# Performance work log

Hardware: AMD Instinct MI355X
Metric: run time of the kernel (lower is better)

The kernel has to match this reference:

```python
import jax, jax.numpy as jnp
import numpy as np

K = 16
EPS = 1e-5
SLOPE = 0.2


def knn_idx(k, xyz_k, xyz_q):
    # xyz_k: (B,Nk,3), xyz_q: (B,Nq,3) -> (B,Nq,k) indices of k nearest in xyz_k
    d = (jnp.sum(xyz_q * xyz_q, -1, keepdims=True)
         - 2.0 * jnp.einsum('bqc,bkc->bqk', xyz_q, xyz_k)
         + jnp.sum(xyz_k * xyz_k, -1)[:, None, :])
    _, idx = jax.lax.top_k(-d, k)
    return idx


def graph_feature(coor_q, x_q, coor_k, x_k):
    # coor_*: (B,N*,3); x_q: (B,C,Nq); x_k: (B,C,Nk) -> (B,2C,Nq,K)
    idx = knn_idx(K, coor_k, coor_q)                      # (B,Nq,K)
    nbr = jax.vmap(lambda xk, i: xk[:, i])(x_k, idx)       # (B,C,Nq,K)
    xq = x_q[:, :, :, None]                                # (B,C,Nq,1)
    xq = jnp.broadcast_to(xq, nbr.shape)
    return jnp.concatenate([nbr - xq, xq], axis=1)


def group_norm(x, gamma, beta, groups=4):
    B, C, N, Kk = x.shape
    xg = x.reshape(B, groups, C // groups, N, Kk)
    mu = jnp.mean(xg, axis=(2, 3, 4), keepdims=True)
    var = jnp.var(xg, axis=(2, 3, 4), keepdims=True)
    xn = ((xg - mu) / jnp.sqrt(var + EPS)).reshape(B, C, N, Kk)
    return xn * gamma[None, :, None, None] + beta[None, :, None, None]


def cgl(f, W, gamma, beta):
    # 1x1 Conv2d (no bias) + GroupNorm(4) + LeakyReLU(0.2)
    y = jnp.einsum('oc,bcnk->bonk', W, f)
    return jax.nn.leaky_relu(group_norm(y, gamma, beta), SLOPE)


def fps(xyz, m):
    # furthest point sampling. xyz: (B,N,3) -> (B,m) int32
    B, N, _ = xyz.shape
    first = jnp.zeros((B,), jnp.int32)

    def body(carry, _):
        dist, last = carry
        lp = jnp.take_along_axis(xyz, last[:, None, None].astype(jnp.int32), axis=1)  # (B,1,3)
        d = jnp.sum((xyz - lp) ** 2, -1)
        dist = jnp.minimum(dist, d)
        nxt = jnp.argmax(dist, -1).astype(jnp.int32)
        return (dist, nxt), nxt

    init = (jnp.full((B, N), 1e10, jnp.float32), first)
    _, rest = jax.lax.scan(body, init, None, length=m - 1)  # (m-1,B)
    return jnp.concatenate([first[None, :], rest], axis=0).T  # (B,m)


def fps_downsample(coor, x, m):
    # coor: (B,N,3), x: (B,C,N) -> new_coor (B,3,m), new_x (B,C,m)
    idx = fps(coor, m)                                        # (B,m)
    new_coor = jnp.take_along_axis(coor, idx[:, :, None], axis=1).transpose(0, 2, 1)
    new_x = jnp.take_along_axis(x, idx[:, None, :], axis=2)
    return new_coor, new_x


def setup_inputs() -> dict:
    key = jax.random.key(0)
    ks = jax.random.split(key, 16)
    d = {
        'x': jax.random.normal(ks[0], (8, 4096, 3), jnp.float32),
        'num0': 2048, 'num1': 512, 'num2': 128,
        'w_in': jax.random.normal(ks[1], (8, 3), jnp.float32) * 0.3,
        'b_in': jnp.zeros((8,), jnp.float32),
    }
    layer_dims = {'1': (32, 16), '2': (64, 64), '4': (128, 128),
                  '5': (128, 256), '6': (256, 256), '7': (256, 512)}
    for i, (name, (o, c)) in enumerate(layer_dims.items()):
        d[f'w{name}'] = jax.random.normal(ks[2 + i], (o, c), jnp.float32) * (1.0 / np.sqrt(c))
        d[f'g{name}'] = jnp.ones((o,), jnp.float32)
        d[f'be{name}'] = jnp.zeros((o,), jnp.float32)
    return d


def reference(x, num0, num1, num2, w_in, b_in,
              w1, g1, be1, w2, g2, be2, w4, g4, be4,
              w5, g5, be5, w6, g6, be6, w7, g7, be7):
    xyz = x.transpose(0, 2, 1)                                # (B,3,N)
    coor = x                                                  # (B,N,3)
    f = jnp.einsum('oc,bcn->bon', w_in, xyz) + b_in[None, :, None]  # (B,8,N)

    f = cgl(graph_feature(coor, f, coor, f), w1, g1, be1)     # (B,32,N,K)
    f = jnp.max(f, axis=-1)                                   # (B,32,N)

    sp1, f_q = fps_downsample(coor, f, num0)                  # (B,3,n0),(B,32,n0)
    coor_d = sp1.transpose(0, 2, 1)                           # (B,n0,3)
    f = cgl(graph_feature(coor_d, f_q, coor, f), w2, g2, be2)
    stage1_feature = jnp.max(f, axis=-1)                      # (B,64,n0)
    coor = coor_d

    sp2, f_q = fps_downsample(coor, stage1_feature, num1)
    coor_d = sp2.transpose(0, 2, 1)
    f = cgl(graph_feature(coor_d, f_q, coor, stage1_feature), w4, g4, be4)
    f = jnp.max(f, axis=-1)                                   # (B,128,n1)
    f = cgl(graph_feature(coor_d, f, coor_d, f), w5, g5, be5)
    stage2_feature = jnp.max(f, axis=-1)                      # (B,128,n1)
    coor = coor_d

    sp3, f_q = fps_downsample(coor, stage2_feature, num2)
    coor_d = sp3.transpose(0, 2, 1)
    f = cgl(graph_feature(coor_d, f_q, coor, stage2_feature), w6, g6, be6)
    f = jnp.max(f, axis=-1)                                   # (B,256,n2)
    f = cgl(graph_feature(coor_d, f, coor_d, f), w7, g7, be7)
    stage3_feature = jnp.max(f, axis=-1)                      # (B,256,n2)

    out_coor = sp3.transpose(0, 2, 1)                         # (B,n2,3)
    out_f = stage3_feature.transpose(0, 2, 1)                 # (B,n2,256)
    return out_coor, out_f
```

## Files before the change

kernel.cpp:

```cpp
#include <hip/hip_runtime.h>
#include <hip/hip_bf16.h>
#include <math.h>

#define DEVI __device__ __forceinline__
typedef unsigned long long ull;

__global__ void k_feat0(const float* __restrict__ x,
                        const float* __restrict__ w_in,
                        const float* __restrict__ b_in,
                        float* __restrict__ coords0, float* __restrict__ feat0,
                        float* __restrict__ stats)
{
  int t = blockIdx.x*blockDim.x + threadIdx.x;
  if (t < 384) stats[t] = 0.f;
  if (t >= 8*4096) return;
  float cx = x[t*3+0], cy = x[t*3+1], cz = x[t*3+2];
  coords0[t*3+0]=cx; coords0[t*3+1]=cy; coords0[t*3+2]=cz;
  #pragma unroll
  for (int o=0;o<8;o++){
    float s = __fadd_rn(__fadd_rn(__fmul_rn(cx,w_in[o*3+0]),
                                  __fmul_rn(cy,w_in[o*3+1])),
                        __fmul_rn(cz,w_in[o*3+2]));
    feat0[t*8+o] = __fadd_rn(s, b_in[o]);
  }
}

template<int CTRL>
DEVI void dppmax64(unsigned& hi, unsigned& lo){
  unsigned oh = (unsigned)__builtin_amdgcn_update_dpp((int)hi,(int)hi,CTRL,0xF,0xF,false);
  unsigned ol = (unsigned)__builtin_amdgcn_update_dpp((int)lo,(int)lo,CTRL,0xF,0xF,false);
  bool tk = (oh > hi) || (oh == hi && ol > lo);
  hi = tk?oh:hi; lo = tk?ol:lo;
}

template<int P>
DEVI void fps_stage(float (&px)[P], float (&py)[P], float (&pz)[P],
                    int m, float sx, float sy, float sz,
                    const float* cpx, const float* cpy, const float* cpz,
                    ull* mK,
                    int* ssel, float* snx, float* sny, float* snz, int tid)
{
  const int wv = tid>>6, lane = tid&63;
  float dist[P];
  #pragma unroll
  for (int p=0;p<P;p++) dist[p]=1e10f;
  if (tid==0){ ssel[0]=0; if (snx){ snx[0]=sx; sny[0]=sy; snz[0]=sz; } }
  #pragma unroll 1
  for (int it=1; it<m; it++){
    float bv = -1.f;
    #pragma unroll
    for (int p=0;p<P;p++){
      float dx=__fsub_rn(px[p],sx);
      float dy=__fsub_rn(py[p],sy);
      float dz=__fsub_rn(pz[p],sz);
      float d = __fadd_rn(__fadd_rn(__fmul_rn(dx,dx),__fmul_rn(dy,dy)),
                          __fmul_rn(dz,dz));
      d = fminf(dist[p], d);
      dist[p] = d;
      bv = fmaxf(bv, d);
    }
    int bidx = 0;
    #pragma unroll
    for (int p=P-1;p>=0;p--) if (dist[p]==bv) bidx = tid+(p<<8);
    const unsigned itu = (unsigned)it;
    unsigned hi = __float_as_uint(bv);
    unsigned lo = ((~(unsigned)bidx & 0xFFFu)<<12) | itu;
    dppmax64<0x111>(hi,lo);
    dppmax64<0x112>(hi,lo);
    dppmax64<0x114>(hi,lo);
    dppmax64<0x118>(hi,lo);
    dppmax64<0x142>(hi,lo);
    dppmax64<0x143>(hi,lo);
    ull* slot = mK + ((it&1)<<2);
    if (lane==63)
      *(volatile ull*)(slot + wv) = ((ull)hi<<32) | (ull)lo;
    ull k0,k1,k2,k3;
    for (;;){
      asm volatile("" ::: "memory");
      k0=slot[0]; k1=slot[1]; k2=slot[2]; k3=slot[3];
      unsigned chk = (((unsigned)k0 ^ itu) | ((unsigned)k1 ^ itu) |
                      ((unsigned)k2 ^ itu) | ((unsigned)k3 ^ itu)) & 0xFFFu;
      if (chk == 0u) break;
    }
    ull ka = (k1>k0)?k1:k0;
    ull kb = (k3>k2)?k3:k2;
    ull kw = (kb>ka)?kb:ka;
    int gi = (int)((~((unsigned)(kw & 0xffffffffull) >> 12)) & 0xFFFu);
    sx = cpx[gi]; sy = cpy[gi]; sz = cpz[gi];
    if (tid==0){
      ssel[it]=gi;
      if (snx){ snx[it]=sx; sny[it]=sy; snz[it]=sz; }
    }
  }
}

template<int CTRL>
DEVI void dppmin_fj(float& d, int& j){
  float od = __int_as_float(__builtin_amdgcn_update_dpp(__float_as_int(d),__float_as_int(d),CTRL,0xF,0xF,false));
  int   oj = __builtin_amdgcn_update_dpp(j,j,CTRL,0xF,0xF,false);
  bool tk = (od < d) || (od == d && oj < j);
  d = tk?od:d; j = tk?oj:j;
}

DEVI float dist_qk(const float* __restrict__ ckb, int j,
                   float qx, float qy, float qz, float sqq){
  float kx=ckb[3*j], ky=ckb[3*j+1], kz=ckb[3*j+2];
  float sk  = __fadd_rn(__fadd_rn(__fmul_rn(kx,kx),__fmul_rn(ky,ky)),
                        __fmul_rn(kz,kz));
  float dot = __fadd_rn(__fadd_rn(__fmul_rn(qx,kx),__fmul_rn(qy,ky)),
                        __fmul_rn(qz,kz));
  return __fadd_rn(__fsub_rn(sqq, __fmul_rn(2.0f,dot)), sk);
}

template<int NPL>
DEVI void knn_wave(const float* __restrict__ cq, int Nq,
                   const float* __restrict__ ck, int Nk,
                   int* __restrict__ idx_out, int b, int q, int lane)
{
  size_t r3 = ((size_t)b*Nq+q)*3;
  float qx=cq[r3], qy=cq[r3+1], qz=cq[r3+2];
  float sqq = __fadd_rn(__fadd_rn(__fmul_rn(qx,qx),__fmul_rn(qy,qy)),
                        __fmul_rn(qz,qz));
  constexpr int GS = (NPL < 8) ? NPL : 8;
  constexpr int NG = NPL / GS;
  float gv[NG]; int gj[NG];
  const float* ckb = ck + (size_t)b*Nk*3;
  ull exmask = 0;
  int dirtyg = -1;
  int myout = 0;
  #pragma unroll 1
  for (int r=0; r<16; r++){
    #pragma unroll
    for (int g=0; g<NG; g++){
      if (dirtyg < 0 || dirtyg == g){
        float nv=__int_as_float(0x7f800000); int nj=0x7fffffff;
        #pragma unroll
        for (int e=0; e<GS; e++){
          const int i = g*GS+e;
          int j = lane + (i<<6);
          float d = dist_qk(ckb, j, qx,qy,qz, sqq);
          bool rem = ((exmask >> i) & 1ull) == 0ull;
          if (rem && d < nv){ nv=d; nj=j; }
        }
        gv[g]=nv; gj[g]=nj;
      }
    }
    float lv = gv[0]; int lj = gj[0];
    #pragma unroll
    for (int g=1; g<NG; g++)
      if (gv[g]<lv || (gv[g]==lv && gj[g]<lj)){ lv=gv[g]; lj=gj[g]; }
    float rd = lv; int rj = lj;
    dppmin_fj<0x111>(rd,rj);
    dppmin_fj<0x112>(rd,rj);
    dppmin_fj<0x114>(rd,rj);
    dppmin_fj<0x118>(rd,rj);
    dppmin_fj<0x142>(rd,rj);
    dppmin_fj<0x143>(rd,rj);
    int wj = __builtin_amdgcn_readlane(rj,63);
    if (lane == r) myout = wj;
    if ((wj & 63) == lane) exmask |= (1ull << (wj>>6));
    dirtyg = (wj>>6)/GS;
  }
  if (lane<16) idx_out[((size_t)b*Nq+q)*16 + lane] = myout;
}

template<int NPL>
__global__ __launch_bounds__(256,3) void k_knn_t(const float* __restrict__ cq, int Nq,
                                                 const float* __restrict__ ck, int Nk,
                                                 int* __restrict__ idx_out)
{
  const int b = blockIdx.y;
  const int q = blockIdx.x*4 + (threadIdx.x>>6);
  if (q >= Nq) return;
  knn_wave<NPL>(cq, Nq, ck, Nk, idx_out, b, q, threadIdx.x&63);
}

__global__ __launch_bounds__(256) void k_fps_knn1(
    const float* __restrict__ coords0,
    int* __restrict__ idx1, int* __restrict__ idx2, int* __restrict__ idx3,
    float* __restrict__ c1, float* __restrict__ c2, float* __restrict__ c3,
    float* __restrict__ out, int* __restrict__ knn1)
{
  __shared__ float s1x[4096], s1y[4096], s1z[4096];
  __shared__ float s2x[2048], s2y[2048], s2z[2048];
  __shared__ float s3x[512],  s3y[512],  s3z[512];
  __shared__ float s4x[128],  s4y[128],  s4z[128];
  __shared__ int   ssel[2048];
  __shared__ alignas(32) ull mK[8];
  if (blockIdx.x >= 8){
    int flat = blockIdx.x - 8;
    int b = flat >> 10, qb = flat & 1023;
    int q = qb*4 + (threadIdx.x>>6);
    knn_wave<64>(coords0, 4096, coords0, 4096, knn1, b, q, threadIdx.x&63);
    return;
  }
  const int b = blockIdx.x, tid = threadIdx.x;
  __builtin_amdgcn_s_setprio(3);
  const float* cb = coords0 + (size_t)b*4096*3;
  if (tid<8) mK[tid] = ~0ull;
  {
    float px[16], py[16], pz[16];
    #pragma unroll
    for (int p=0;p<16;p++){
      int j = tid + (p<<8);
      float X=cb[3*j], Y=cb[3*j+1], Z=cb[3*j+2];
      px[p]=X; py[p]=Y; pz[p]=Z;
      s1x[j]=X; s1y[j]=Y; s1z[j]=Z;
    }
    float sx=cb[0], sy=cb[1], sz=cb[2];
    __syncthreads();
    fps_stage<16>(px,py,pz, 2048, sx,sy,sz, s1x,s1y,s1z,
                  mK, ssel, s2x,s2y,s2z, tid);
  }
  __syncthreads();
  {
    float* c1b = c1 + (size_t)b*2048*3;
    for (int i=tid;i<2048;i+=256){
      idx1[b*2048+i]=ssel[i];
      c1b[3*i]=s2x[i]; c1b[3*i+1]=s2y[i]; c1b[3*i+2]=s2z[i];
    }
  }
  {
    float px[8], py[8], pz[8];
    #pragma unroll
    for (int p=0;p<8;p++){
      int j = tid + (p<<8);
      px[p]=s2x[j]; py[p]=s2y[j]; pz[p]=s2z[j];
    }
    float sx=s2x[0], sy=s2y[0], sz=s2z[0];
    __syncthreads();
    fps_stage<8>(px,py,pz, 512, sx,sy,sz, s2x,s2y,s2z,
                 mK, ssel, s3x,s3y,s3z, tid);
  }
  __syncthreads();
  {
    float* c2b = c2 + (size_t)b*512*3;
    for (int i=tid;i<512;i+=256){
      idx2[b*512+i]=ssel[i];
      c2b[3*i]=s3x[i]; c2b[3*i+1]=s3y[i]; c2b[3*i+2]=s3z[i];
    }
  }
  {
    float px[2], py[2], pz[2];
    #pragma unroll
    for (int p=0;p<2;p++){
      int j = tid + (p<<8);
      px[p]=s3x[j]; py[p]=s3y[j]; pz[p]=s3z[j];
    }
    float sx=s3x[0], sy=s3y[0], sz=s3z[0];
    __syncthreads();
    fps_stage<2>(px,py,pz, 128, sx,sy,sz, s3x,s3y,s3z,
                 mK, ssel, s4x,s4y,s4z, tid);
  }
  __syncthreads();
  {
    float* c3b = c3 + (size_t)b*128*3;
    float* ob  = out + (size_t)b*128*3;
    for (int i=tid;i<128;i+=256){
      idx3[b*128+i]=ssel[i];
      float X=s4x[i],Y=s4y[i],Z=s4z[i];
      c3b[3*i]=X; c3b[3*i+1]=Y; c3b[3*i+2]=Z;
      ob[3*i]=X; ob[3*i+1]=Y; ob[3*i+2]=Z;
    }
  }
}

struct WtParams {
  const float* W[6];
  float* wl[6];
  float* wq[6];
  int O[6], C[6], OC[6];
};
__global__ void k_wt_all(WtParams p){
  int s = blockIdx.y;
  int t = blockIdx.x*blockDim.x + threadIdx.x;
  int OC = p.OC[s];
  if (t >= OC) return;
  int C = p.C[s], O = p.O[s];
  int o = t / C, c = t - o*C;
  const float* W = p.W[s];
  float wlv = W[o*2*C + c];
  float wrv = W[o*2*C + C + c];
  p.wl[s][c*O+o] = wlv;
  p.wq[s][c*O+o] = wrv - wlv;
}

#define GEMM_M 8
__global__ void k_gemm_dual(const float* __restrict__ feat, int Nk, int C, int O,
                            const float* __restrict__ wlT, const float* __restrict__ wqT,
                            float* __restrict__ yk, float* __restrict__ yq)
{
  extern __shared__ float sf[];
  const int b = blockIdx.y;
  const int o = threadIdx.x & (O-1);
  const int rg = threadIdx.x / O;
  const int R = blockDim.x / O;
  const int rowsPB = R*GEMM_M;
  const int row0 = blockIdx.x * rowsPB;
  const int Cp = C+1;
  const float* src = feat + ((size_t)b*Nk + row0)*C;
  for (int i=threadIdx.x; i<rowsPB*C; i+=blockDim.x){
    int r = i / C, c = i - r*C;
    sf[r*Cp + c] = src[i];
  }
  __syncthreads();
  float ak[GEMM_M], aq[GEMM_M];
  #pragma unroll
  for (int m=0;m<GEMM_M;m++){ ak[m]=0.f; aq[m]=0.f; }
  const float* lp = wlT + o;
  const float* qp = wqT + o;
  const float* sfr = sf + rg*GEMM_M*Cp;
  for (int c=0;c<C;c++){
    float wl = lp[(size_t)c*O];
    float wq = qp[(size_t)c*O];
    #pragma unroll
    for (int m=0;m<GEMM_M;m++){
      float xv = sfr[m*Cp + c];
      ak[m] = fmaf(xv, wl, ak[m]);
      aq[m] = fmaf(xv, wq, aq[m]);
    }
  }
  size_t obase = ((size_t)b*Nk + row0 + rg*GEMM_M)*O + o;
  #pragma unroll
  for (int m=0;m<GEMM_M;m++){
    yk[obase + (size_t)m*O] = ak[m];
    yq[obase + (size_t)m*O] = aq[m];
  }
}

__global__ void k_gather(const float* __restrict__ yk, const float* __restrict__ yq,
                         const int* __restrict__ knnidx, const int* __restrict__ qmap,
                         int Nq, int Nk, int O,
                         float* __restrict__ vmax, float* __restrict__ stats)
{
  const int b = blockIdx.y;
  const int o = threadIdx.x & (O-1);
  const int rg = threadIdx.x / O;
  const int R = blockDim.x / O;
  float ls=0.f, ls2=0.f;
  const float* ykb = yk + (size_t)b*Nk*O;
  const float* yqb = yq + (size_t)b*Nk*O;
  for (int nq = blockIdx.x*R + rg; nq < Nq; nq += gridDim.x*R){
    int qj = qmap ? qmap[b*Nq+nq] : nq;
    float vq = yqb[(size_t)qj*O + o];
    const int* ip = knnidx + ((size_t)b*Nq+nq)*16;
    float vmx = -3.4e38f;
    #pragma unroll
    for (int k=0;k<16;k++){
      int j = ip[k];
      float v = ykb[(size_t)j*O+o] + vq;
      vmx = fmaxf(vmx, v);
      ls += v; ls2 = fmaf(v,v,ls2);
    }
    vmax[((size_t)b*Nq+nq)*O+o] = vmx;
  }
  int span = O/4; if (span>64) span=64;
  for (int mm=1; mm<span; mm<<=1){
    ls  += __shfl_xor(ls, mm);
    ls2 += __shfl_xor(ls2, mm);
  }
  __shared__ float sred[8];
  if (threadIdx.x<8) sred[threadIdx.x]=0.f;
  __syncthreads();
  int lane = threadIdx.x & 63;
  if ((lane & (span-1))==0){
    int g = (o*4)/O;
    atomicAdd(&sred[g*2+0], ls);
    atomicAdd(&sred[g*2+1], ls2);
  }
  __syncthreads();
  if (threadIdx.x<8) atomicAdd(&stats[b*8+threadIdx.x], sred[threadIdx.x]);
}

__global__ void k_norm(const float* __restrict__ vmax, const float* __restrict__ stats,
                       const float* __restrict__ gamma,
                       const float* __restrict__ beta,
                       int Nq, int O, float invcnt, float* __restrict__ outf)
{
  const int b = blockIdx.y;
  const int n = Nq*O;
  for (int i = blockIdx.x*blockDim.x+threadIdx.x; i<n; i+=gridDim.x*blockDim.x){
    int o = i & (O-1);
    int g = (o*4)/O;
    float s1 = stats[b*8+g*2], s2 = stats[b*8+g*2+1];
    float mu = s1*invcnt;
    float var = fmaf(-mu,mu, s2*invcnt);
    float rs = 1.0f/sqrtf(var+1e-5f);
    float v = (vmax[(size_t)b*n + i]-mu)*rs*gamma[o] + beta[o];
    outf[(size_t)b*n + i] = (v>=0.f)? v : 0.2f*v;
  }
}

extern "C" void kernel_launch(void* const* d_in, const int* in_sizes, int n_in,
                              void* d_out, int out_size, void* d_ws, size_t ws_size,
                              hipStream_t stream)
{
  const int B = 8;
  const float* x    = (const float*)d_in[0];
  const float* w_in = (const float*)d_in[4];
  const float* b_in = (const float*)d_in[5];
  const float *Wm[6], *Gm[6], *Bm[6];
  for (int i=0;i<6;i++){
    Wm[i]=(const float*)d_in[6+3*i];
    Gm[i]=(const float*)d_in[6+3*i+1];
    Bm[i]=(const float*)d_in[6+3*i+2];
  }
  float* ws = (float*)d_ws;
  float* out = (float*)d_out;
  const size_t OFF_C0=0,        OFF_F0=98304,   OFF_F1=360448,  OFF_F2=1409024,
               OFF_F4=2457600,  OFF_F5=2981888, OFF_F6=3506176, OFF_F7=3768320,
               OFF_C1=4030464,  OFF_C2=4079616, OFF_C3=4091904,
               OFF_YK=4094976,  OFF_YQ=6192128, OFF_VM=8289280,
               OFF_WL=9337856,  OFF_WQ=9468928, OFF_ST=9600000,
               OFF_I1=9600384,  OFF_I2=9616768, OFF_I3=9620864, OFF_KNN=9621888,
               TOTAL=10146176;
  if (ws_size < TOTAL*sizeof(float)) return;
  float *c0=ws+OFF_C0, *f0=ws+OFF_F0, *f1=ws+OFF_F1, *f2=ws+OFF_F2,
        *f4=ws+OFF_F4, *f5=ws+OFF_F5, *f6=ws+OFF_F6,
        *c1=ws+OFF_C1, *c2=ws+OFF_C2, *c3=ws+OFF_C3,
        *yk=ws+OFF_YK, *yq=ws+OFF_YQ, *vm=ws+OFF_VM, *stats=ws+OFF_ST;
  int *i1=(int*)(ws+OFF_I1), *i2=(int*)(ws+OFF_I2), *i3=(int*)(ws+OFF_I3),
      *knn=(int*)(ws+OFF_KNN);

  const int OCs[6]  = {256, 2048, 8192, 16384, 32768, 65536};
  const int OCoff[6]= {0,   256,  2304, 10496, 26880, 59648};

  struct St { int C,O,Nk,Nq; const float* feat; const float* cq; const float* ck;
              const int* qmap; float* outf; };
  const St st[6] = {
    {8,   32, 4096, 4096, f0, c0, c0, nullptr, f1},
    {32,  64, 4096, 2048, f1, c1, c0, i1,      f2},
    {64, 128, 2048,  512, f2, c2, c1, i2,      f4},
    {128,128,  512,  512, f4, c2, c2, nullptr, f5},
    {128,256,  512,  128, f5, c3, c2, i3,      f6},
    {256,256,  128,  128, f6, c3, c3, nullptr, out + 8*128*3},
  };

  k_feat0 <<<(8*4096+255)/256, 256, 0, stream>>>(x, w_in, b_in, c0, f0, stats);

  WtParams wp;
  for (int s=0;s<6;s++){
    wp.W[s]=Wm[s];
    wp.wl[s]=ws+OFF_WL+OCoff[s];
    wp.wq[s]=ws+OFF_WQ+OCoff[s];
    wp.O[s]=st[s].O; wp.C[s]=st[s].C; wp.OC[s]=OCs[s];
  }
  k_wt_all<<<dim3(256,6), 256, 0, stream>>>(wp);

  k_fps_knn1<<<8 + 8*1024, 256, 0, stream>>>(c0, i1, i2, i3, c1, c2, c3,
                                             out, knn);

  for (int s=0;s<6;s++){
    const St& S = st[s];
    if (s > 0){
      dim3 gk((S.Nq + 3)/4, B);
      int npl = S.Nk >> 6;
      if      (npl == 64) k_knn_t<64><<<gk, 256, 0, stream>>>(S.cq, S.Nq, S.ck, S.Nk, knn);
      else if (npl == 32) k_knn_t<32><<<gk, 256, 0, stream>>>(S.cq, S.Nq, S.ck, S.Nk, knn);
      else if (npl ==  8) k_knn_t< 8><<<gk, 256, 0, stream>>>(S.cq, S.Nq, S.ck, S.Nk, knn);
      else                k_knn_t< 2><<<gk, 256, 0, stream>>>(S.cq, S.Nq, S.ck, S.Nk, knn);
    }
    int rowsPB = 2048 / S.O;
    dim3 gg(S.Nk / rowsPB, B);
    size_t shb = (size_t)rowsPB * (S.C+1) * sizeof(float);
    k_gemm_dual<<<gg, 256, shb, stream>>>(S.feat, S.Nk, S.C, S.O,
                                          ws+OFF_WL+OCoff[s], ws+OFF_WQ+OCoff[s],
                                          yk, yq);
    dim3 gs(64, B);
    k_gather<<<gs, 256, 0, stream>>>(yk, yq, knn, S.qmap, S.Nq, S.Nk, S.O,
                                     vm, stats + s*64);
    float invcnt = 1.0f / ((float)(S.O/4) * (float)S.Nq * 16.0f);
    dim3 gn((S.Nq*S.O + 255)/256, B);
    k_norm<<<gn, 256, 0, stream>>>(vm, stats + s*64, Gm[s], Bm[s],
                                   S.Nq, S.O, invcnt, S.outf);
  }
}
```

Baseline: 2.564 ms.

## Pack two batch FPS chains per 512-thread block with interleaved shared coords

The fused FPS+kNN kernel now runs two independent batch FPS chains in one 512-thread block, each 256-thread half using its own mailbox and buffers. Stage-1 coordinates are gathered straight from global memory instead of being staged in shared memory. Shared coordinate buffers switch from split x/y/z arrays to interleaved xyz, so copy-outs become flat contiguous loops. The kNN part of the launch is regrouped into 512-thread blocks of 8 queries. This cuts shared-memory use and the number of FPS blocks, but the two chains now share block-wide __syncthreads and a compute unit, and each serial step reads its selected point from global memory.

```diff
diff --git a/kernel.cpp b/kernel.cpp
--- a/kernel.cpp
+++ b/kernel.cpp
@@ -36,15 +36,15 @@
 template<int P>
 DEVI void fps_stage(float (&px)[P], float (&py)[P], float (&pz)[P],
                     int m, float sx, float sy, float sz,
-                    const float* cpx, const float* cpy, const float* cpz,
-                    ull* mK,
-                    int* ssel, float* snx, float* sny, float* snz, int tid)
-{
-  const int wv = tid>>6, lane = tid&63;
+                    const float* cp,
+                    ull* mK8,
+                    int* ssel, float* sn, int ltid)
+{
+  const int wv = ltid>>6, lane = ltid&63;
   float dist[P];
   #pragma unroll
   for (int p=0;p<P;p++) dist[p]=1e10f;
-  if (tid==0){ ssel[0]=0; if (snx){ snx[0]=sx; sny[0]=sy; snz[0]=sz; } }
+  if (ltid==0){ ssel[0]=0; sn[0]=sx; sn[1]=sy; sn[2]=sz; }
   #pragma unroll 1
   for (int it=1; it<m; it++){
     float bv = -1.f;
@@ -61,7 +61,7 @@
     }
     int bidx = 0;
     #pragma unroll
-    for (int p=P-1;p>=0;p--) if (dist[p]==bv) bidx = tid+(p<<8);
+    for (int p=P-1;p>=0;p--) if (dist[p]==bv) bidx = ltid+(p<<8);
     const unsigned itu = (unsigned)it;
     unsigned hi = __float_as_uint(bv);
     unsigned lo = ((~(unsigned)bidx & 0xFFFu)<<12) | itu;
@@ -71,7 +71,7 @@
     dppmax64<0x118>(hi,lo);
     dppmax64<0x142>(hi,lo);
     dppmax64<0x143>(hi,lo);
-    ull* slot = mK + ((it&1)<<2);
+    ull* slot = mK8 + ((it&1)<<2);
     if (lane==63)
       *(volatile ull*)(slot + wv) = ((ull)hi<<32) | (ull)lo;
     ull k0,k1,k2,k3;
@@ -86,10 +86,10 @@
     ull kb = (k3>k2)?k3:k2;
     ull kw = (kb>ka)?kb:ka;
     int gi = (int)((~((unsigned)(kw & 0xffffffffull) >> 12)) & 0xFFFu);
-    sx = cpx[gi]; sy = cpy[gi]; sz = cpz[gi];
-    if (tid==0){
+    sx = cp[3*gi]; sy = cp[3*gi+1]; sz = cp[3*gi+2];
+    if (ltid==0){
       ssel[it]=gi;
-      if (snx){ snx[it]=sx; sny[it]=sy; snz[it]=sz; }
+      sn[3*it]=sx; sn[3*it+1]=sy; sn[3*it+2]=sz;
     }
   }
 }
@@ -175,93 +175,81 @@
   knn_wave<NPL>(cq, Nq, ck, Nk, idx_out, b, q, threadIdx.x&63);
 }
 
-__global__ __launch_bounds__(256) void k_fps_knn1(
+__global__ __launch_bounds__(512) void k_fps_knn1(
     const float* __restrict__ coords0,
     int* __restrict__ idx1, int* __restrict__ idx2, int* __restrict__ idx3,
     float* __restrict__ c1, float* __restrict__ c2, float* __restrict__ c3,
     float* __restrict__ out, int* __restrict__ knn1)
 {
-  __shared__ float s1x[4096], s1y[4096], s1z[4096];
-  __shared__ float s2x[2048], s2y[2048], s2z[2048];
-  __shared__ float s3x[512],  s3y[512],  s3z[512];
-  __shared__ float s4x[128],  s4y[128],  s4z[128];
-  __shared__ int   ssel[2048];
-  __shared__ alignas(32) ull mK[8];
-  if (blockIdx.x >= 8){
-    int flat = blockIdx.x - 8;
-    int b = flat >> 10, qb = flat & 1023;
-    int q = qb*4 + (threadIdx.x>>6);
+  __shared__ float s2[2][2048*3];
+  __shared__ float s3[2][512*3];
+  __shared__ float s4[2][128*3];
+  __shared__ int   ssel[2][2048];
+  __shared__ ull   mK[2][8];
+  if (blockIdx.x >= 4){
+    int flat = blockIdx.x - 4;
+    int b = flat >> 9, qb = flat & 511;
+    int q = qb*8 + (threadIdx.x>>6);
     knn_wave<64>(coords0, 4096, coords0, 4096, knn1, b, q, threadIdx.x&63);
     return;
   }
-  const int b = blockIdx.x, tid = threadIdx.x;
+  const int tid = threadIdx.x;
+  const int g = tid>>8, ltid = tid&255;
+  const int b = blockIdx.x*2 + g;
   __builtin_amdgcn_s_setprio(3);
   const float* cb = coords0 + (size_t)b*4096*3;
-  if (tid<8) mK[tid] = ~0ull;
+  if (tid<16) mK[tid>>3][tid&7] = ~0ull;
   {
     float px[16], py[16], pz[16];
     #pragma unroll
     for (int p=0;p<16;p++){
-      int j = tid + (p<<8);
-      float X=cb[3*j], Y=cb[3*j+1], Z=cb[3*j+2];
-      px[p]=X; py[p]=Y; pz[p]=Z;
-      s1x[j]=X; s1y[j]=Y; s1z[j]=Z;
+      int j = ltid + (p<<8);
+      px[p]=cb[3*j]; py[p]=cb[3*j+1]; pz[p]=cb[3*j+2];
     }
     float sx=cb[0], sy=cb[1], sz=cb[2];
     __syncthreads();
-    fps_stage<16>(px,py,pz, 2048, sx,sy,sz, s1x,s1y,s1z,
-                  mK, ssel, s2x,s2y,s2z, tid);
+    fps_stage<16>(px,py,pz, 2048, sx,sy,sz, cb, mK[g], ssel[g], s2[g], ltid);
   }
   __syncthreads();
   {
     float* c1b = c1 + (size_t)b*2048*3;
-    for (int i=tid;i<2048;i+=256){
-      idx1[b*2048+i]=ssel[i];
-      c1b[3*i]=s2x[i]; c1b[3*i+1]=s2y[i]; c1b[3*i+2]=s2z[i];
-    }
+    for (int i=ltid;i<2048;i+=256) idx1[b*2048+i]=ssel[g][i];
+    for (int i=ltid;i<2048*3;i+=256) c1b[i]=s2[g][i];
   }
   {
     float px[8], py[8], pz[8];
     #pragma unroll
     for (int p=0;p<8;p++){
-      int j = tid + (p<<8);
-      px[p]=s2x[j]; py[p]=s2y[j]; pz[p]=s2z[j];
-    }
-    float sx=s2x[0], sy=s2y[0], sz=s2z[0];
+      int j = ltid + (p<<8);
+      px[p]=s2[g][3*j]; py[p]=s2[g][3*j+1]; pz[p]=s2[g][3*j+2];
+    }
+    float sx=s2[g][0], sy=s2[g][1], sz=s2[g][2];
     __syncthreads();
-    fps_stage<8>(px,py,pz, 512, sx,sy,sz, s2x,s2y,s2z,
-                 mK, ssel, s3x,s3y,s3z, tid);
+    fps_stage<8>(px,py,pz, 512, sx,sy,sz, s2[g], mK[g], ssel[g], s3[g], ltid);
   }
   __syncthreads();
   {
     float* c2b = c2 + (size_t)b*512*3;
-    for (int i=tid;i<512;i+=256){
-      idx2[b*512+i]=ssel[i];
-      c2b[3*i]=s3x[i]; c2b[3*i+1]=s3y[i]; c2b[3*i+2]=s3z[i];
-    }
+    for (int i=ltid;i<512;i+=256) idx2[b*512+i]=ssel[g][i];
+    for (int i=ltid;i<512*3;i+=256) c2b[i]=s3[g][i];
   }
   {
     float px[2], py[2], pz[2];
     #pragma unroll
     for (int p=0;p<2;p++){
-      int j = tid + (p<<8);
-      px[p]=s3x[j]; py[p]=s3y[j]; pz[p]=s3z[j];
-    }
-    float sx=s3x[0], sy=s3y[0], sz=s3z[0];
+      int j = ltid + (p<<8);
+      px[p]=s3[g][3*j]; py[p]=s3[g][3*j+1]; pz[p]=s3[g][3*j+2];
+    }
+    float sx=s3[g][0], sy=s3[g][1], sz=s3[g][2];
     __syncthreads();
-    fps_stage<2>(px,py,pz, 128, sx,sy,sz, s3x,s3y,s3z,
-                 mK, ssel, s4x,s4y,s4z, tid);
+    fps_stage<2>(px,py,pz, 128, sx,sy,sz, s3[g], mK[g], ssel[g], s4[g], ltid);
   }
   __syncthreads();
   {
     float* c3b = c3 + (size_t)b*128*3;
     float* ob  = out + (size_t)b*128*3;
-    for (int i=tid;i<128;i+=256){
-      idx3[b*128+i]=ssel[i];
-      float X=s4x[i],Y=s4y[i],Z=s4z[i];
-      c3b[3*i]=X; c3b[3*i+1]=Y; c3b[3*i+2]=Z;
-      ob[3*i]=X; ob[3*i+1]=Y; ob[3*i+2]=Z;
-    }
+    for (int i=ltid;i<128;i+=256) idx3[b*128+i]=ssel[g][i];
+    for (int i=ltid;i<128*3;i+=256){ float v=s4[g][i]; c3b[i]=v; ob[i]=v; }
   }
 }
 
@@ -447,8 +435,8 @@
   }
   k_wt_all<<<dim3(256,6), 256, 0, stream>>>(wp);
 
-  k_fps_knn1<<<8 + 8*1024, 256, 0, stream>>>(c0, i1, i2, i3, c1, c2, c3,
-                                             out, knn);
+  k_fps_knn1<<<4 + 8*512, 512, 0, stream>>>(c0, i1, i2, i3, c1, c2, c3,
+                                            out, knn);
 
   for (int s=0;s<6;s++){
     const St& S = st[s];
```

After: 3.108 ms. 21.2% more time.
